# Kernel optimization log

Hardware: AMD Instinct MI355X
Metric: run time of the kernel (lower is better)

Reference implementation:

```python
import jax, jax.numpy as jnp
import numpy as np

B, T, C = 4, 2048, 1024
H = 16
D = C // H  # 64


def setup_inputs() -> dict:
    key = jax.random.key(0)
    k1, k2, k3 = jax.random.split(key, 3)
    x = jax.random.normal(k1, (B, T, C), dtype=jnp.float32)
    W_attn = jax.random.normal(k2, (C, 3 * C), dtype=jnp.float32) * (1.0 / np.sqrt(C))
    W_proj = jax.random.normal(k3, (C, C), dtype=jnp.float32) * (1.0 / np.sqrt(C))
    return {"x": x, "W_attn": W_attn, "W_proj": W_proj}


def reference(x, W_attn, W_proj):
    b, t, c = x.shape
    # qkv projection: [B,T,3C]
    qkv = jnp.einsum('btc,cd->btd', x, W_attn)
    q, k, v = jnp.split(qkv, 3, axis=-1)
    # split heads -> [B,H,T,D]
    q = q.reshape(b, t, H, D).transpose(0, 2, 1, 3)
    k = k.reshape(b, t, H, D).transpose(0, 2, 1, 3)
    v = v.reshape(b, t, H, D).transpose(0, 2, 1, 3)
    # scores scaled by 1/sqrt(C) (faithful to source: uses full embed dim)
    att = jnp.einsum('bhtd,bhsd->bhts', q, k) * (1.0 / jnp.sqrt(jnp.float32(c)))
    # causal mask: -inf where key index > query index
    causal = jnp.tril(jnp.ones((t, t), dtype=bool))
    att = jnp.where(causal, att, jnp.float32(-jnp.inf))
    att = jax.nn.softmax(att, axis=-1)
    # attention output -> combine heads
    y = jnp.einsum('bhts,bhsd->bhtd', att, v)
    y = y.transpose(0, 2, 1, 3).reshape(b, t, c)
    z = jnp.einsum('btc,cd->btd', y, W_proj)
    return z
```

## Files before the change

kernel.cpp:

```cpp
#include <hip/hip_runtime.h>
#include <hip/hip_bf16.h>

typedef __bf16 bf16x8 __attribute__((ext_vector_type(8)));
typedef float f32x4 __attribute__((ext_vector_type(4)));

static __device__ __forceinline__ __bf16 tobf(float x) {
    __hip_bfloat16 h = __float2bfloat16(x);
    __bf16 r;
    __builtin_memcpy(&r, &h, 2);
    return r;
}

static __device__ __forceinline__ float fexp2(float x) {
    float r;
    asm("v_exp_f32 %0, %1" : "=v"(r) : "v"(x));
    return r;
}

__global__ __launch_bounds__(256) void prep_k(const float* __restrict__ x,
                                              __hip_bfloat16* __restrict__ x_bf,
                                              const float* __restrict__ Wa,
                                              __hip_bfloat16* __restrict__ WaT,
                                              const float* __restrict__ Wp,
                                              __hip_bfloat16* __restrict__ WpT) {
    __shared__ float tile[32][33];
    const int bid = blockIdx.x;
    const int tid = threadIdx.x;
    if (bid < 8192) {
        int i = bid * 256 + tid;
        float4 v = reinterpret_cast<const float4*>(x)[i];
        __hip_bfloat16 a = __float2bfloat16(v.x);
        __hip_bfloat16 b = __float2bfloat16(v.y);
        __hip_bfloat16 c = __float2bfloat16(v.z);
        __hip_bfloat16 d = __float2bfloat16(v.w);
        ushort4 o;
        o.x = *reinterpret_cast<unsigned short*>(&a);
        o.y = *reinterpret_cast<unsigned short*>(&b);
        o.z = *reinterpret_cast<unsigned short*>(&c);
        o.w = *reinterpret_cast<unsigned short*>(&d);
        reinterpret_cast<ushort4*>(x_bf)[i] = o;
        return;
    }
    const float* in;
    __hip_bfloat16* out;
    int bx, Cn, qrows;
    float qscale;
    int t;
    if (bid < 8192 + 3072) {
        t = bid - 8192;
        in = Wa; out = WaT; Cn = 3072; qrows = 1024;
        qscale = 0.045084223f;
        bx = t % 96;
    } else {
        t = bid - 11264;
        in = Wp; out = WpT; Cn = 1024; qrows = 0;
        qscale = 1.0f;
        bx = t % 32;
    }
    const int by = (bid < 11264) ? (t / 96) : (t / 32);
    const int R = 1024;
    const int c0 = bx * 32, r0 = by * 32;
    const int tx = tid & 31, ty = tid >> 5;
#pragma unroll
    for (int i = 0; i < 4; ++i)
        tile[ty + i * 8][tx] = in[(size_t)(r0 + ty + i * 8) * Cn + c0 + tx];
    __syncthreads();
#pragma unroll
    for (int i = 0; i < 4; ++i) {
        int orow = c0 + ty + i * 8;
        float v = tile[tx][ty + i * 8];
        if (orow < qrows) v *= qscale;
        out[(size_t)orow * R + r0 + tx] = __float2bfloat16(v);
    }
}

__global__ __launch_bounds__(256) void vtrans_k(const __hip_bfloat16* __restrict__ qkv,
                                                __hip_bfloat16* __restrict__ Vt) {
    __shared__ __attribute__((aligned(16))) __hip_bfloat16 lds[64 * 72];
    const int tt = blockIdx.x;
    const int bh = blockIdx.y;
    const int b = bh >> 4, h = bh & 15;
    const int tid = threadIdx.x;
    const __hip_bfloat16* src =
        qkv + (size_t)b * 2048 * 3072 + 2048 + h * 64 + (size_t)tt * 64 * 3072;
#pragma unroll
    for (int p = 0; p < 2; ++p) {
        int u = p * 256 + tid;
        int t_in = u >> 3, dc = u & 7;
        bf16x8 v = *reinterpret_cast<const bf16x8*>(src + (size_t)t_in * 3072 + dc * 8);
        *reinterpret_cast<bf16x8*>(&lds[t_in * 72 + dc * 8]) = v;
    }
    __syncthreads();
    __hip_bfloat16* dst = Vt + (size_t)bh * 64 * 2048 + tt * 64;
#pragma unroll
    for (int p = 0; p < 2; ++p) {
        int w = p * 256 + tid;
        int d = w >> 3, oc = w & 7;
        bf16x8 o;
#pragma unroll
        for (int e = 0; e < 8; ++e) {
            int s = oc * 8 + e;
            int r = (s & 3) | (((s >> 3) & 3) << 2) | (((s >> 2) & 1) << 4);
            int t_in = (s & 32) | r;
            o[e] = lds[t_in * 72 + d];
        }
        *reinterpret_cast<bf16x8*>(&dst[(size_t)d * 2048 + oc * 8]) = o;
    }
}

template <bool OUT_BF16>
__global__ __launch_bounds__(256, 2) void gemm4w(const __hip_bfloat16* __restrict__ A,
                                                 const __hip_bfloat16* __restrict__ Bt,
                                                 __hip_bfloat16* __restrict__ Cb,
                                                 float* __restrict__ Cf,
                                                 int M, int N, int K) {
    __shared__ __attribute__((aligned(16))) char As[2][128 * 128];
    __shared__ __attribute__((aligned(16))) char Bs[2][128 * 128];
    const int tid = threadIdx.x;
    const int lane = tid & 63, wid = tid >> 6;
    const int l15 = lane & 15, lg = lane >> 4;
    const int wr = wid >> 1, wc = wid & 1;
    const int lin = blockIdx.y * gridDim.x + blockIdx.x;
    const int cpx = (gridDim.x * gridDim.y) >> 3;
    const int sw = (lin & 7) * cpx + (lin >> 3);
    const int bn = sw % gridDim.x, bm = sw / gridDim.x;
    const size_t arow0 = (size_t)bm * 128;
    const size_t brow0 = (size_t)bn * 128;

    f32x4 acc[4][4] = {};

    const __hip_bfloat16* pa[4];
    const __hip_bfloat16* pb[4];
#pragma unroll
    for (int p = 0; p < 4; ++p) {
        int idx = p * 256 + tid;
        int row = idx >> 3, c = idx & 7;
        int col = 8 * (c ^ (row & 7));
        pa[p] = A + (arow0 + row) * (size_t)K + col;
        pb[p] = Bt + (brow0 + row) * (size_t)K + col;
    }

    auto stage = [&](int buf) {
        char* Ad = buf ? &As[1][0] : &As[0][0];
        char* Bd = buf ? &Bs[1][0] : &Bs[0][0];
#pragma unroll
        for (int p = 0; p < 4; ++p) {
            __builtin_amdgcn_global_load_lds(
                (const __attribute__((address_space(1))) void*)pa[p],
                (__attribute__((address_space(3))) void*)(Ad + (p * 256 + tid) * 16), 16, 0, 0);
            __builtin_amdgcn_global_load_lds(
                (const __attribute__((address_space(1))) void*)pb[p],
                (__attribute__((address_space(3))) void*)(Bd + (p * 256 + tid) * 16), 16, 0, 0);
            pa[p] += 64;
            pb[p] += 64;
        }
    };

    stage(0);
    asm volatile("s_waitcnt vmcnt(0)" ::: "memory");
    __syncthreads();

    const int nk = K >> 6;
    int cur = 0;
    for (int kt = 0; kt < nk; ++kt) {
        if (kt + 1 < nk) stage(cur ^ 1);
        const char* Ab = cur ? &As[1][0] : &As[0][0];
        const char* Bb = cur ? &Bs[1][0] : &Bs[0][0];
#pragma unroll
        for (int ks = 0; ks < 2; ++ks) {
            bf16x8 af[4], bfr[4];
#pragma unroll
            for (int mf = 0; mf < 4; ++mf) {
                int R = wr * 64 + mf * 16 + l15;
                af[mf] = *reinterpret_cast<const bf16x8*>(
                    Ab + R * 128 + 16 * ((ks * 4 + lg) ^ (R & 7)));
            }
#pragma unroll
            for (int nf = 0; nf < 4; ++nf) {
                int R = wc * 64 + nf * 16 + l15;
                bfr[nf] = *reinterpret_cast<const bf16x8*>(
                    Bb + R * 128 + 16 * ((ks * 4 + lg) ^ (R & 7)));
            }
            __builtin_amdgcn_s_setprio(1);
#pragma unroll
            for (int mf = 0; mf < 4; ++mf)
#pragma unroll
                for (int nf = 0; nf < 4; ++nf)
                    acc[mf][nf] = __builtin_amdgcn_mfma_f32_16x16x32_bf16(af[mf], bfr[nf],
                                                                          acc[mf][nf], 0, 0, 0);
            __builtin_amdgcn_s_setprio(0);
        }
        asm volatile("s_waitcnt vmcnt(0)" ::: "memory");
        __syncthreads();
        cur ^= 1;
    }

#pragma unroll
    for (int mf = 0; mf < 4; ++mf) {
#pragma unroll
        for (int nf = 0; nf < 4; ++nf) {
#pragma unroll
            for (int j = 0; j < 4; ++j) {
                int row = bm * 128 + wr * 64 + mf * 16 + lg * 4 + j;
                int col = bn * 128 + wc * 64 + nf * 16 + l15;
                if (OUT_BF16)
                    Cb[(size_t)row * N + col] = __float2bfloat16(acc[mf][nf][j]);
                else
                    Cf[(size_t)row * N + col] = acc[mf][nf][j];
            }
        }
    }
}

__global__ __launch_bounds__(256) void attn_k(const __hip_bfloat16* __restrict__ qkv,
                                              const __hip_bfloat16* __restrict__ Vt,
                                              __hip_bfloat16* __restrict__ y) {
    constexpr int TT = 2048;
    constexpr int S3C = 3072;
    const int bh = blockIdx.x, b = bh >> 4, h = bh & 15;
    const int st = 15 - (int)blockIdx.y;
    const int tid = threadIdx.x;
    const int wid = tid >> 6, lane = tid & 63;
    const int l15 = lane & 15, lg = lane >> 4;

    __shared__ __attribute__((aligned(16))) char Ks[2][64 * 128];
    __shared__ __attribute__((aligned(16))) char Vs[2][64 * 128];

    const __hip_bfloat16* base = qkv + (size_t)b * TT * S3C;
    const int qo = h * 64, ko = 1024 + h * 64;
    const __hip_bfloat16* vt = Vt + (size_t)bh * 64 * TT;

    bf16x8 vones;
#pragma unroll
    for (int i = 0; i < 8; ++i) vones[i] = tobf(1.0f);

    const int idx0 = tid, idx1 = 256 + tid;
    const int r0 = idx0 >> 3, c0 = 8 * ((idx0 & 7) ^ (r0 & 7));
    const int r1 = idx1 >> 3, c1 = 8 * ((idx1 & 7) ^ (r1 & 7));

    const int qbase = st * 128 + wid * 32;
    const int my_nt = (qbase >> 6) + 1;
    const int blk_nt = st * 2 + 2;

    bf16x8 aq[2][2];
#pragma unroll
    for (int m = 0; m < 2; ++m) {
        const __hip_bfloat16* qp = base + (size_t)(qbase + m * 16 + l15) * S3C + qo + lg * 8;
        aq[m][0] = *reinterpret_cast<const bf16x8*>(qp);
        aq[m][1] = *reinterpret_cast<const bf16x8*>(qp + 32);
    }

    f32x4 acc[2][4] = {};
    f32x4 lsum[2] = {};

    const __hip_bfloat16* kp0 = base + (size_t)r0 * S3C + ko + c0;
    const __hip_bfloat16* kp1 = base + (size_t)r1 * S3C + ko + c1;
    const __hip_bfloat16* vp0 = vt + (size_t)r0 * TT + c0;
    const __hip_bfloat16* vp1 = vt + (size_t)r1 * TT + c1;

    auto stage = [&](int buf) {
        char* Kd = buf ? &Ks[1][0] : &Ks[0][0];
        char* Vd = buf ? &Vs[1][0] : &Vs[0][0];
        __builtin_amdgcn_global_load_lds(
            (const __attribute__((address_space(1))) void*)kp0,
            (__attribute__((address_space(3))) void*)(Kd + idx0 * 16), 16, 0, 0);
        __builtin_amdgcn_global_load_lds(
            (const __attribute__((address_space(1))) void*)kp1,
            (__attribute__((address_space(3))) void*)(Kd + idx1 * 16), 16, 0, 0);
        __builtin_amdgcn_global_load_lds(
            (const __attribute__((address_space(1))) void*)vp0,
            (__attribute__((address_space(3))) void*)(Vd + idx0 * 16), 16, 0, 0);
        __builtin_amdgcn_global_load_lds(
            (const __attribute__((address_space(1))) void*)vp1,
            (__attribute__((address_space(3))) void*)(Vd + idx1 * 16), 16, 0, 0);
        kp0 += (size_t)64 * S3C;
        kp1 += (size_t)64 * S3C;
        vp0 += 64;
        vp1 += 64;
    };

    stage(0);
    asm volatile("s_waitcnt vmcnt(0)" ::: "memory");
    __syncthreads();

    int cur = 0;
    for (int kt = 0; kt < blk_nt; ++kt) {
        if (kt + 1 < blk_nt) stage(cur ^ 1);
        if (kt < my_nt) {
            const int kb = kt * 64;
            const char* Kb = cur ? &Ks[1][0] : &Ks[0][0];
            const char* Vb = cur ? &Vs[1][0] : &Vs[0][0];
            const int swl = l15 & 7;
            f32x4 s[2][4];
            __builtin_amdgcn_s_setprio(1);
#pragma unroll
            for (int cg = 0; cg < 4; ++cg) {
                const char* krow = Kb + (cg * 16 + l15) * 128;
                bf16x8 k0 = *reinterpret_cast<const bf16x8*>(krow + 16 * (lg ^ swl));
                bf16x8 k1 = *reinterpret_cast<const bf16x8*>(krow + 16 * ((4 + lg) ^ swl));
#pragma unroll
                for (int m = 0; m < 2; ++m) {
                    f32x4 z = {0.f, 0.f, 0.f, 0.f};
                    z = __builtin_amdgcn_mfma_f32_16x16x32_bf16(k0, aq[m][0], z, 0, 0, 0);
                    z = __builtin_amdgcn_mfma_f32_16x16x32_bf16(k1, aq[m][1], z, 0, 0, 0);
                    s[m][cg] = z;
                }
            }
            __builtin_amdgcn_s_setprio(0);
            bf16x8 vb[2][4];
#pragma unroll
            for (int dg = 0; dg < 4; ++dg) {
                const char* vrow = Vb + (dg * 16 + l15) * 128;
                vb[0][dg] = *reinterpret_cast<const bf16x8*>(vrow + 16 * (lg ^ swl));
                vb[1][dg] = *reinterpret_cast<const bf16x8*>(vrow + 16 * ((4 + lg) ^ swl));
            }
            float p[2][4][4];
            const bool needmask = (kb + 63 > qbase);
#pragma unroll
            for (int m = 0; m < 2; ++m)
#pragma unroll
                for (int cg = 0; cg < 4; ++cg)
#pragma unroll
                    for (int j = 0; j < 4; ++j) {
                        float e = fexp2(s[m][cg][j]);
                        if (needmask) {
                            int key = kb + cg * 16 + lg * 4 + j;
                            int qrow = qbase + m * 16 + l15;
                            e = (key > qrow) ? 0.f : e;
                        }
                        p[m][cg][j] = e;
                    }
            bf16x8 pa[2][2];
#pragma unroll
            for (int m = 0; m < 2; ++m)
#pragma unroll
                for (int ks = 0; ks < 2; ++ks) {
                    bf16x8 tt2;
                    tt2[0] = tobf(p[m][2 * ks][0]);
                    tt2[1] = tobf(p[m][2 * ks][1]);
                    tt2[2] = tobf(p[m][2 * ks][2]);
                    tt2[3] = tobf(p[m][2 * ks][3]);
                    tt2[4] = tobf(p[m][2 * ks + 1][0]);
                    tt2[5] = tobf(p[m][2 * ks + 1][1]);
                    tt2[6] = tobf(p[m][2 * ks + 1][2]);
                    tt2[7] = tobf(p[m][2 * ks + 1][3]);
                    pa[m][ks] = tt2;
                }
            __builtin_amdgcn_s_setprio(1);
#pragma unroll
            for (int ks = 0; ks < 2; ++ks) {
#pragma unroll
                for (int dg = 0; dg < 4; ++dg)
#pragma unroll
                    for (int m = 0; m < 2; ++m)
                        acc[m][dg] = __builtin_amdgcn_mfma_f32_16x16x32_bf16(
                            pa[m][ks], vb[ks][dg], acc[m][dg], 0, 0, 0);
#pragma unroll
                for (int m = 0; m < 2; ++m)
                    lsum[m] = __builtin_amdgcn_mfma_f32_16x16x32_bf16(pa[m][ks], vones,
                                                                      lsum[m], 0, 0, 0);
            }
            __builtin_amdgcn_s_setprio(0);
        }
        asm volatile("s_waitcnt vmcnt(0)" ::: "memory");
        __syncthreads();
        cur ^= 1;
    }

#pragma unroll
    for (int m = 0; m < 2; ++m)
#pragma unroll
        for (int j = 0; j < 4; ++j) {
            float inv = 1.f / lsum[m][j];
            int t = qbase + m * 16 + lg * 4 + j;
#pragma unroll
            for (int dg = 0; dg < 4; ++dg) {
                float o = acc[m][dg][j] * inv;
                y[((size_t)(b * TT + t)) * 1024 + h * 64 + dg * 16 + l15] = __float2bfloat16(o);
            }
        }
}

extern "C" void kernel_launch(void* const* d_in, const int* in_sizes, int n_in,
                              void* d_out, int out_size, void* d_ws, size_t ws_size,
                              hipStream_t stream) {
    const float* x = (const float*)d_in[0];
    const float* Wa = (const float*)d_in[1];
    const float* Wp = (const float*)d_in[2];
    float* out = (float*)d_out;

    __hip_bfloat16* ws = (__hip_bfloat16*)d_ws;
    __hip_bfloat16* x_bf = ws;
    __hip_bfloat16* WaT = x_bf + (size_t)8192 * 1024;
    __hip_bfloat16* WpT = WaT + (size_t)3072 * 1024;
    __hip_bfloat16* qkv = WpT + (size_t)1024 * 1024;
    __hip_bfloat16* ybf = qkv + (size_t)8192 * 3072;
    __hip_bfloat16* Vt = ybf + (size_t)8192 * 1024;

    prep_k<<<8192 + 3072 + 1024, 256, 0, stream>>>(x, x_bf, Wa, WaT, Wp, WpT);
    gemm4w<true><<<dim3(24, 64), 256, 0, stream>>>(x_bf, WaT, qkv, nullptr, 8192, 3072, 1024);
    vtrans_k<<<dim3(32, 64), 256, 0, stream>>>(qkv, Vt);
    attn_k<<<dim3(64, 16), 256, 0, stream>>>(qkv, Vt, ybf);
    gemm4w<false><<<dim3(8, 64), 256, 0, stream>>>(ybf, WpT, nullptr, out, 8192, 1024, 1024);
}
```

Measured before the change: 165.6 us.

## Fuse V transpose into QKV GEMM epilogue, drop separate vtrans kernel

The QKV projection GEMM now handles the V-column tiles differently: it stages accumulators through LDS and writes them straight out in the permuted transposed Vt layout, skipping the row-major store. The separate vtrans kernel goes away, along with one launch and a global write plus read of V. In exchange the V-tile epilogue needs two LDS passes with extra barriers and narrow 2-byte LDS accesses, so those blocks run longer than the others.

```diff
diff --git a/kernel.cpp b/kernel.cpp
--- a/kernel.cpp
+++ b/kernel.cpp
@@ -74,45 +74,12 @@
     }
 }
 
-__global__ __launch_bounds__(256) void vtrans_k(const __hip_bfloat16* __restrict__ qkv,
-                                                __hip_bfloat16* __restrict__ Vt) {
-    __shared__ __attribute__((aligned(16))) __hip_bfloat16 lds[64 * 72];
-    const int tt = blockIdx.x;
-    const int bh = blockIdx.y;
-    const int b = bh >> 4, h = bh & 15;
-    const int tid = threadIdx.x;
-    const __hip_bfloat16* src =
-        qkv + (size_t)b * 2048 * 3072 + 2048 + h * 64 + (size_t)tt * 64 * 3072;
-#pragma unroll
-    for (int p = 0; p < 2; ++p) {
-        int u = p * 256 + tid;
-        int t_in = u >> 3, dc = u & 7;
-        bf16x8 v = *reinterpret_cast<const bf16x8*>(src + (size_t)t_in * 3072 + dc * 8);
-        *reinterpret_cast<bf16x8*>(&lds[t_in * 72 + dc * 8]) = v;
-    }
-    __syncthreads();
-    __hip_bfloat16* dst = Vt + (size_t)bh * 64 * 2048 + tt * 64;
-#pragma unroll
-    for (int p = 0; p < 2; ++p) {
-        int w = p * 256 + tid;
-        int d = w >> 3, oc = w & 7;
-        bf16x8 o;
-#pragma unroll
-        for (int e = 0; e < 8; ++e) {
-            int s = oc * 8 + e;
-            int r = (s & 3) | (((s >> 3) & 3) << 2) | (((s >> 2) & 1) << 4);
-            int t_in = (s & 32) | r;
-            o[e] = lds[t_in * 72 + d];
-        }
-        *reinterpret_cast<bf16x8*>(&dst[(size_t)d * 2048 + oc * 8]) = o;
-    }
-}
-
-template <bool OUT_BF16>
+template <bool OUT_BF16, bool FUSE_VT>
 __global__ __launch_bounds__(256, 2) void gemm4w(const __hip_bfloat16* __restrict__ A,
                                                  const __hip_bfloat16* __restrict__ Bt,
                                                  __hip_bfloat16* __restrict__ Cb,
                                                  float* __restrict__ Cf,
+                                                 __hip_bfloat16* __restrict__ VtOut,
                                                  int M, int N, int K) {
     __shared__ __attribute__((aligned(16))) char As[2][128 * 128];
     __shared__ __attribute__((aligned(16))) char Bs[2][128 * 128];
@@ -193,6 +160,48 @@
         asm volatile("s_waitcnt vmcnt(0)" ::: "memory");
         __syncthreads();
         cur ^= 1;
+    }
+
+    if (FUSE_VT && bn >= 16) {
+        const int trow0 = bm * 128;
+        const int b = trow0 >> 11;
+        const int t0 = trow0 & 2047;
+        const int cv0 = bn * 128 - 2048;
+        __hip_bfloat16* lds = reinterpret_cast<__hip_bfloat16*>(&As[0][0]);
+#pragma unroll 1
+        for (int pass = 0; pass < 2; ++pass) {
+            __syncthreads();
+            if (wr == pass) {
+#pragma unroll
+                for (int mf = 0; mf < 4; ++mf)
+#pragma unroll
+                    for (int nf = 0; nf < 4; ++nf)
+#pragma unroll
+                        for (int j = 0; j < 4; ++j) {
+                            int rloc = mf * 16 + lg * 4 + j;
+                            int col = wc * 64 + nf * 16 + l15;
+                            lds[rloc * 136 + col] = __float2bfloat16(acc[mf][nf][j]);
+                        }
+            }
+            __syncthreads();
+#pragma unroll
+            for (int q = 0; q < 4; ++q) {
+                int u = q * 256 + tid;
+                int vr = u >> 3, oc = u & 7;
+                bf16x8 o;
+#pragma unroll
+                for (int e = 0; e < 8; ++e) {
+                    int s = oc * 8 + e;
+                    int slot = s & 31;
+                    int r = (slot & 3) | (((slot >> 3) & 3) << 2) | (((slot >> 2) & 1) << 4);
+                    int tsrc = (s & 32) | r;
+                    o[e] = tobf(__bfloat162float(lds[tsrc * 136 + vr]));
+                }
+                size_t vrow = (size_t)b * 1024 + cv0 + vr;
+                *reinterpret_cast<bf16x8*>(&VtOut[vrow * 2048 + t0 + pass * 64 + oc * 8]) = o;
+            }
+        }
+        return;
     }
 
 #pragma unroll
@@ -398,8 +407,9 @@
     __hip_bfloat16* Vt = ybf + (size_t)8192 * 1024;
 
     prep_k<<<8192 + 3072 + 1024, 256, 0, stream>>>(x, x_bf, Wa, WaT, Wp, WpT);
-    gemm4w<true><<<dim3(24, 64), 256, 0, stream>>>(x_bf, WaT, qkv, nullptr, 8192, 3072, 1024);
-    vtrans_k<<<dim3(32, 64), 256, 0, stream>>>(qkv, Vt);
+    gemm4w<true, true><<<dim3(24, 64), 256, 0, stream>>>(x_bf, WaT, qkv, nullptr, Vt,
+                                                         8192, 3072, 1024);
     attn_k<<<dim3(64, 16), 256, 0, stream>>>(qkv, Vt, ybf);
-    gemm4w<false><<<dim3(8, 64), 256, 0, stream>>>(ybf, WpT, nullptr, out, 8192, 1024, 1024);
-}
+    gemm4w<false, false><<<dim3(8, 64), 256, 0, stream>>>(ybf, WpT, nullptr, out, nullptr,
+                                                          8192, 1024, 1024);
+}
```

Result: faster. 160.2 us (median of 2 runs) (-3.3%).
